# Kernel optimization log

Hardware: AMD Instinct MI355X
Metric: run time of the kernel (lower is better)

## Reference

```python
import jax, jax.numpy as jnp
import numpy as np

NUM_ENTITIES = 50000
NUM_FEATURES = 64
NUM_RELATIONS = 500
BATCH = 64


def setup_inputs() -> dict:
    key = jax.random.key(0)
    k1, k2, k3, k4, k5, k6 = jax.random.split(key, 6)
    numerical_literals = jax.random.normal(k1, (NUM_ENTITIES, NUM_FEATURES), dtype=jnp.float32)
    c = jax.random.normal(k2, (NUM_FEATURES,), dtype=jnp.float32)
    # variance must be positive; uniform in [0.5, 1.5)
    var = jax.random.uniform(k3, (NUM_FEATURES,), dtype=jnp.float32) + 0.5
    nf_weights = jax.random.normal(k4, (NUM_RELATIONS, NUM_FEATURES), dtype=jnp.float32)
    head_ids = jax.random.randint(k5, (BATCH,), 0, NUM_ENTITIES, dtype=jnp.int64)
    rel_ids = jax.random.randint(k6, (BATCH,), 0, NUM_RELATIONS, dtype=jnp.int64)
    return {
        "numerical_literals": numerical_literals,
        "c": c,
        "var": var,
        "nf_weights": nf_weights,
        "head_ids": head_ids,
        "rel_ids": rel_ids,
    }


def reference(numerical_literals, c, var, nf_weights, head_ids, rel_ids):
    # head_literals: [B, F]
    head_lit = numerical_literals[head_ids]
    # literal_diff: [B, E, F] broadcast subtraction (the large intermediate)
    diff = head_lit[:, None, :] - numerical_literals[None, :, :]
    # RBF: exp(-(n - c)^2 / var), c/var broadcast over feature dim
    phi = jnp.exp(-jnp.square(diff - c) / var)
    # per-relation feature weights: [B, F]
    w = nf_weights[rel_ids]
    # bmm(phi, w[...,None]).squeeze(-1) -> [B, E]
    return jnp.einsum("bef,bf->be", phi, w)
```

## Files before the change

### kernel.cpp

```cpp
#include <hip/hip_runtime.h>
#include <hip/hip_bf16.h>

#define E_TOT 50000
#define NF    64
#define B_TOT 64
#define B_TILE 8
#define BLOCK 256

__global__ __launch_bounds__(BLOCK, 8)
void kbln_kernel(const float* __restrict__ NL,
                 const float* __restrict__ c,
                 const float* __restrict__ varr,
                 const float* __restrict__ NFW,
                 const int*   __restrict__ head_ids,
                 const int*   __restrict__ rel_ids,
                 float*       __restrict__ out)
{
    __shared__ float sQ[NF];
    __shared__ float4 sA[B_TILE][NF / 4];
    __shared__ float4 sW[B_TILE][NF / 4];

    const int tid = threadIdx.x;
    const int b0  = blockIdx.y * B_TILE;
    const int e   = blockIdx.x * BLOCK + tid;

    if (tid < NF) {
        sQ[tid] = sqrtf(1.4426950408889634f / varr[tid]);
    }
    __syncthreads();

    for (int i = tid; i < B_TILE * NF; i += BLOCK) {
        const int bi = i >> 6;
        const int f  = i & (NF - 1);
        const int h  = head_ids[b0 + bi];
        const int r  = rel_ids[b0 + bi];
        reinterpret_cast<float*>(&sA[bi][0])[f] =
            (NL[(size_t)h * NF + f] - c[f]) * sQ[f];
        reinterpret_cast<float*>(&sW[bi][0])[f] = NFW[(size_t)r * NF + f];
    }
    __syncthreads();

    if (e >= E_TOT) return;

    const float4* nl4 = reinterpret_cast<const float4*>(NL + (size_t)e * NF);
    const float4* q4  = reinterpret_cast<const float4*>(sQ);

    float acc[B_TILE];
#pragma unroll
    for (int bi = 0; bi < B_TILE; ++bi) acc[bi] = 0.0f;

#pragma unroll
    for (int i = 0; i < NF / 4; ++i) {
        const float4 v = nl4[i];
        const float4 q = q4[i];
        float4 n;
        n.x = v.x * q.x; n.y = v.y * q.y; n.z = v.z * q.z; n.w = v.w * q.w;
#pragma unroll
        for (int bi = 0; bi < B_TILE; ++bi) {
            const float4 a = sA[bi][i];
            const float4 w = sW[bi][i];
            float t;
            t = a.x - n.x; acc[bi] = fmaf(__builtin_amdgcn_exp2f(-(t * t)), w.x, acc[bi]);
            t = a.y - n.y; acc[bi] = fmaf(__builtin_amdgcn_exp2f(-(t * t)), w.y, acc[bi]);
            t = a.z - n.z; acc[bi] = fmaf(__builtin_amdgcn_exp2f(-(t * t)), w.z, acc[bi]);
            t = a.w - n.w; acc[bi] = fmaf(__builtin_amdgcn_exp2f(-(t * t)), w.w, acc[bi]);
        }
    }

#pragma unroll
    for (int bi = 0; bi < B_TILE; ++bi) {
        out[(size_t)(b0 + bi) * E_TOT + e] = acc[bi];
    }
}

extern "C" void kernel_launch(void* const* d_in, const int* in_sizes, int n_in,
                              void* d_out, int out_size, void* d_ws, size_t ws_size,
                              hipStream_t stream)
{
    const float* NL       = (const float*)d_in[0];
    const float* c        = (const float*)d_in[1];
    const float* varr     = (const float*)d_in[2];
    const float* NFW      = (const float*)d_in[3];
    const int*   head_ids = (const int*)d_in[4];
    const int*   rel_ids  = (const int*)d_in[5];
    float*       out      = (float*)d_out;

    dim3 grid((E_TOT + BLOCK - 1) / BLOCK, B_TOT / B_TILE);
    kbln_kernel<<<grid, dim3(BLOCK), 0, stream>>>(NL, c, varr, NFW, head_ids, rel_ids, out);
}
```

Before: 39.64 us.

## Precompute per-batch head/weight vectors in a prep kernel, read via scalar loads

Moves the head-literal normalization and relation-weight gather into a separate small prep kernel that writes an interleaved A/W table into workspace. The main kernel drops its shared-memory staging and two barriers, reading the table directly from global memory with block-uniform addresses the compiler can turn into scalar loads. This avoids redundant per-block gather work and LDS traffic, but adds a second kernel launch and relies on the uniform loads hitting cache.

```diff
diff --git a/kernel.cpp b/kernel.cpp
--- a/kernel.cpp
+++ b/kernel.cpp
@@ -6,64 +6,67 @@
 #define B_TOT 64
 #define B_TILE 8
 #define BLOCK 256
+#define NCHUNK (NF / 4)
+
+#define WS_Q_OFF (B_TOT * NCHUNK * 8)
+
+__global__ void prep_kernel(const float* __restrict__ NL,
+                            const float* __restrict__ c,
+                            const float* __restrict__ varr,
+                            const float* __restrict__ NFW,
+                            const int*   __restrict__ head_ids,
+                            const int*   __restrict__ rel_ids,
+                            float*       __restrict__ ws)
+{
+    const int idx = blockIdx.x * 256 + threadIdx.x;
+    if (idx < NF) {
+        ws[WS_Q_OFF + idx] = sqrtf(1.4426950408889634f / varr[idx]);
+    }
+    if (idx < B_TOT * NF) {
+        const int b = idx >> 6;
+        const int f = idx & (NF - 1);
+        const float q = sqrtf(1.4426950408889634f / varr[f]);
+        const int h = head_ids[b];
+        const int r = rel_ids[b];
+        const float a = (NL[(size_t)h * NF + f] - c[f]) * q;
+        const float w = NFW[(size_t)r * NF + f];
+        const int i = f >> 2, j = f & 3;
+        ws[((b * NCHUNK + i) << 3) + j]     = a;
+        ws[((b * NCHUNK + i) << 3) + 4 + j] = w;
+    }
+}
 
 __global__ __launch_bounds__(BLOCK, 8)
 void kbln_kernel(const float* __restrict__ NL,
-                 const float* __restrict__ c,
-                 const float* __restrict__ varr,
-                 const float* __restrict__ NFW,
-                 const int*   __restrict__ head_ids,
-                 const int*   __restrict__ rel_ids,
+                 const float* __restrict__ AW,
                  float*       __restrict__ out)
 {
-    __shared__ float sQ[NF];
-    __shared__ float4 sA[B_TILE][NF / 4];
-    __shared__ float4 sW[B_TILE][NF / 4];
-
     const int tid = threadIdx.x;
     const int b0  = blockIdx.y * B_TILE;
     const int e   = blockIdx.x * BLOCK + tid;
-
-    if (tid < NF) {
-        sQ[tid] = sqrtf(1.4426950408889634f / varr[tid]);
-    }
-    __syncthreads();
-
-    for (int i = tid; i < B_TILE * NF; i += BLOCK) {
-        const int bi = i >> 6;
-        const int f  = i & (NF - 1);
-        const int h  = head_ids[b0 + bi];
-        const int r  = rel_ids[b0 + bi];
-        reinterpret_cast<float*>(&sA[bi][0])[f] =
-            (NL[(size_t)h * NF + f] - c[f]) * sQ[f];
-        reinterpret_cast<float*>(&sW[bi][0])[f] = NFW[(size_t)r * NF + f];
-    }
-    __syncthreads();
-
     if (e >= E_TOT) return;
 
     const float4* nl4 = reinterpret_cast<const float4*>(NL + (size_t)e * NF);
-    const float4* q4  = reinterpret_cast<const float4*>(sQ);
+    const float4* q4  = reinterpret_cast<const float4*>(AW + WS_Q_OFF);
 
     float acc[B_TILE];
 #pragma unroll
     for (int bi = 0; bi < B_TILE; ++bi) acc[bi] = 0.0f;
 
 #pragma unroll
-    for (int i = 0; i < NF / 4; ++i) {
+    for (int i = 0; i < NCHUNK; ++i) {
         const float4 v = nl4[i];
         const float4 q = q4[i];
         float4 n;
         n.x = v.x * q.x; n.y = v.y * q.y; n.z = v.z * q.z; n.w = v.w * q.w;
 #pragma unroll
         for (int bi = 0; bi < B_TILE; ++bi) {
-            const float4 a = sA[bi][i];
-            const float4 w = sW[bi][i];
+            const float* aw = AW + (((size_t)(b0 + bi) * NCHUNK + i) << 3);
             float t;
-            t = a.x - n.x; acc[bi] = fmaf(__builtin_amdgcn_exp2f(-(t * t)), w.x, acc[bi]);
-            t = a.y - n.y; acc[bi] = fmaf(__builtin_amdgcn_exp2f(-(t * t)), w.y, acc[bi]);
-            t = a.z - n.z; acc[bi] = fmaf(__builtin_amdgcn_exp2f(-(t * t)), w.z, acc[bi]);
-            t = a.w - n.w; acc[bi] = fmaf(__builtin_amdgcn_exp2f(-(t * t)), w.w, acc[bi]);
+            t = aw[0] - n.x; acc[bi] = fmaf(__builtin_amdgcn_exp2f(-(t * t)), aw[4], acc[bi]);
+            t = aw[1] - n.y; acc[bi] = fmaf(__builtin_amdgcn_exp2f(-(t * t)), aw[5], acc[bi]);
+            t = aw[2] - n.z; acc[bi] = fmaf(__builtin_amdgcn_exp2f(-(t * t)), aw[6], acc[bi]);
+            t = aw[3] - n.w; acc[bi] = fmaf(__builtin_amdgcn_exp2f(-(t * t)), aw[7], acc[bi]);
         }
     }
 
@@ -83,8 +86,12 @@
     const float* NFW      = (const float*)d_in[3];
     const int*   head_ids = (const int*)d_in[4];
     const int*   rel_ids  = (const int*)d_in[5];
+    float*       ws       = (float*)d_ws;
     float*       out      = (float*)d_out;
 
+    prep_kernel<<<dim3(16), dim3(256), 0, stream>>>(NL, c, varr, NFW,
+                                                    head_ids, rel_ids, ws);
+
     dim3 grid((E_TOT + BLOCK - 1) / BLOCK, B_TOT / B_TILE);
-    kbln_kernel<<<grid, dim3(BLOCK), 0, stream>>>(NL, c, varr, NFW, head_ids, rel_ids, out);
+    kbln_kernel<<<grid, dim3(BLOCK), 0, stream>>>(NL, ws, out);
 }
```

After: 52.92 us. +33.5%, slower.
